# Performance work log

Measured on AMD Instinct MI355X. Metric: run time of the kernel, lower is better.

The kernel has to match this reference:

```python
import jax, jax.numpy as jnp
import numpy as np

B, N, D = 2, 2048, 1024
H, HD = 16, 64
BASE = 10000.0
INIT_STD = 0.02


def apply_rope(x, base=BASE):
    """Rotary embedding on the last dim; seq axis is axis 1.

    Works for q of shape (b, n, h, d) and k of shape (b, n, d).
    """
    d = x.shape[-1]
    n = x.shape[1]
    half = d // 2
    inv_freq = 1.0 / (base ** (jnp.arange(half, dtype=jnp.float32) / half))
    ang = jnp.arange(n, dtype=jnp.float32)[:, None] * inv_freq  # (n, d/2)
    extra = x.ndim - 3  # axes between seq axis and feature axis
    ang = ang.reshape((n,) + (1,) * extra + (half,))
    cos, sin = jnp.cos(ang), jnp.sin(ang)
    x1, x2 = jnp.split(x, 2, axis=-1)
    return jnp.concatenate([x1 * cos - x2 * sin, x2 * cos + x1 * sin], axis=-1)


def setup_inputs() -> dict:
    key = jax.random.key(0)
    kx, k1, k2, k3, k4 = jax.random.split(key, 5)
    x = jax.random.normal(kx, (B, N, D), dtype=jnp.float32)
    Wq = jax.random.normal(k1, (D, H * HD), dtype=jnp.float32) * INIT_STD
    Wkv = jax.random.normal(k2, (D, 2 * HD), dtype=jnp.float32) * INIT_STD
    Wkvh = jax.random.normal(k3, (D, 2 * H), dtype=jnp.float32) * INIT_STD
    Wo = jax.random.normal(k4, (H * HD, D), dtype=jnp.float32) * INIT_STD
    return {"x": x, "Wq": Wq, "Wkv": Wkv, "Wkvh": Wkvh, "Wo": Wo}


def reference(x, Wq, Wkv, Wkvh, Wo):
    b, n, d = x.shape
    q = (x @ Wq).reshape(b, n, H, HD)          # (b,n,h,hd)
    kv = x @ Wkv                                # (b,n,2*hd)
    kv_head = jax.nn.sigmoid(x @ Wkvh)          # (b,n,2*h)
    k, v = jnp.split(kv, 2, axis=-1)            # each (b,n,hd)
    k_head, v_head = jnp.split(kv_head, 2, axis=-1)  # each (b,n,h)

    # LRPE (rotary) on q and on the shared low-rank k
    q = apply_rope(q)
    k = apply_rope(k)

    # outer-product expansion: (b,n,h) x (b,n,hd) -> (b,n,h,hd)
    k = jnp.einsum('bnh,bnd->bnhd', k_head, k)
    v = jnp.einsum('bnh,bnd->bnhd', v_head, v)

    # causal softmax attention, scale = 1/sqrt(head_dim)
    scale = 1.0 / np.sqrt(HD)
    scores = jnp.einsum('bqhd,bkhd->bhqk', q, k) * scale
    mask = jnp.tril(jnp.ones((n, n), dtype=bool))
    scores = jnp.where(mask, scores, jnp.finfo(scores.dtype).min)
    p = jax.nn.softmax(scores, axis=-1)
    out = jnp.einsum('bhqk,bkhd->bqhd', p, v)   # (b,n,h,hd)

    out = out.reshape(b, n, H * HD)
    return out @ Wo
```

## Files before the change

### kernel.cpp

```cpp
#include <hip/hip_runtime.h>

typedef unsigned short u16;
typedef unsigned int u32;
typedef __attribute__((ext_vector_type(8))) short short8;
typedef __attribute__((ext_vector_type(4))) float f32x4;
typedef __attribute__((ext_vector_type(4))) u32 u32x4;
typedef __attribute__((ext_vector_type(2))) u32 u32x2;
typedef __attribute__((ext_vector_type(4))) u16 u16x4;

constexpr int B_ = 2, N_ = 2048, H_ = 16;
constexpr int ROWS = B_ * N_;
constexpr float LOG2E = 1.44269504088896f;

__device__ __forceinline__ float bf2f(u16 u){ union{u32 u; float f;} v; v.u = ((u32)u)<<16; return v.f; }
__device__ __forceinline__ u16 f2bf(float f){
  union{float f; u32 u;} v; v.f = f;
  u32 u = v.u; u += 0x7fffu + ((u>>16)&1u);
  return (u16)(u>>16);
}
__device__ __forceinline__ u32 cvtpk(float lo, float hi){
  u32 r; asm("v_cvt_pk_bf16_f32 %0, %1, %2" : "=v"(r) : "v"(lo), "v"(hi)); return r;
}

__global__ __launch_bounds__(256) void k_setup(const float* __restrict__ x, u16* __restrict__ xb,
                                               float2* __restrict__ tab,
                                               const float* __restrict__ Wq, const float* __restrict__ Wo,
                                               u16* __restrict__ WqT, u16* __restrict__ WoT,
                                               const float* __restrict__ Wkv, const float* __restrict__ Wkvh,
                                               u16* __restrict__ WkvT){
  __shared__ float T[64*65];
  int bid = blockIdx.x, tid = threadIdx.x;
  if (bid < 4096){
    int i = (bid*256 + tid)*4;
    f32x4 v = *(const f32x4*)(x + i);
    u16x4 o; o[0]=f2bf(v[0]); o[1]=f2bf(v[1]); o[2]=f2bf(v[2]); o[3]=f2bf(v[3]);
    *(u16x4*)(xb + i) = o;
    return;
  }
  if (bid < 4352){
    int idx = (bid-4096)*256 + tid;
    int i = idx & 31, n = idx >> 5;
    float ang = (float)n * exp2f(-(float)i * 0.4152410118609203f);
    tab[idx] = make_float2(cosf(ang), sinf(ang));
    return;
  }
  if (bid < 4864){
    int m = (bid - 4352) >> 8;
    const float* in = m ? Wo : Wq;
    u16* out = m ? WoT : WqT;
    int t2 = (bid - 4352) & 255;
    int n0 = (t2 & 15) << 6, k0 = (t2 >> 4) << 6;
    #pragma unroll
    for (int s=0; s<4; ++s){
      int chunk = tid + s*256, r = chunk >> 4, c4 = (chunk & 15) << 2;
      *(f32x4*)(&T[r*65 + c4]) = *(const f32x4*)(&in[(size_t)(k0 + r)*1024 + n0 + c4]);
    }
    __syncthreads();
    #pragma unroll
    for (int s=0; s<2; ++s){
      int chunk = tid + s*256, d = chunk >> 3, c8 = (chunk & 7) << 3;
      u16x4 o1, o2;
      #pragma unroll
      for (int j=0; j<4; ++j){ o1[j] = f2bf(T[(c8+j)*65 + d]); o2[j] = f2bf(T[(c8+4+j)*65 + d]); }
      *(u16x4*)(&out[(size_t)(n0 + d)*1024 + k0 + c8])     = o1;
      *(u16x4*)(&out[(size_t)(n0 + d)*1024 + k0 + c8 + 4]) = o2;
    }
    return;
  }
  {
    int idx = (bid - 4864)*256 + tid;
    int n = idx >> 10, k = idx & 1023;
    float v = 0.f;
    if (n < 128)      v = Wkv[k*128 + n];
    else if (n < 160) v = Wkvh[k*32 + (n-128)];
    WkvT[idx] = f2bf(v);
  }
}

__global__ __launch_bounds__(256) void k_gemm_bt(const u16* __restrict__ A, const u16* __restrict__ Bt,
                                                 float* __restrict__ C, int M, int N, int K){
  __shared__ u16 As[64*72];
  __shared__ u16 Bs[64*72];
  int ntile = N >> 6;
  int m0 = (blockIdx.x / ntile) << 6;
  int n0 = (blockIdx.x % ntile) << 6;
  int tid = threadIdx.x;
  int w = tid >> 6, l = tid & 63, lr = l & 15, lc = l >> 4;
  int wm = (w >> 1) * 32, wn = (w & 1) * 32;
  f32x4 acc[2][2] = {};
  for (int kt = 0; kt < K; kt += 64){
    __syncthreads();
    #pragma unroll
    for (int s = 0; s < 2; ++s){
      int chunk = tid + s*256;
      int r = chunk >> 3, c8 = (chunk & 7) << 3;
      *(u32x4*)(&As[r*72 + c8]) = *(const u32x4*)(&A[(size_t)(m0 + r)*K + kt + c8]);
      *(u32x4*)(&Bs[r*72 + c8]) = *(const u32x4*)(&Bt[(size_t)(n0 + r)*K + kt + c8]);
    }
    __syncthreads();
    short8 af[2][2], bfr[2][2];
    #pragma unroll
    for (int mf=0; mf<2; ++mf)
      #pragma unroll
      for (int c=0; c<2; ++c)
        af[mf][c] = *(const short8*)(&As[(wm + mf*16 + lr)*72 + c*32 + lc*8]);
    #pragma unroll
    for (int nf=0; nf<2; ++nf)
      #pragma unroll
      for (int c=0; c<2; ++c)
        bfr[nf][c] = *(const short8*)(&Bs[(wn + nf*16 + lr)*72 + c*32 + lc*8]);
    #pragma unroll
    for (int mf=0; mf<2; ++mf)
      #pragma unroll
      for (int nf=0; nf<2; ++nf)
        #pragma unroll
        for (int c=0; c<2; ++c)
          acc[mf][nf] = __builtin_amdgcn_mfma_f32_16x16x32_bf16(af[mf][c], bfr[nf][c], acc[mf][nf], 0,0,0);
  }
  #pragma unroll
  for (int mf=0; mf<2; ++mf)
    #pragma unroll
    for (int nf=0; nf<2; ++nf)
      #pragma unroll
      for (int r=0; r<4; ++r)
        C[(size_t)(m0 + wm + mf*16 + lc*4 + r)*N + n0 + wn + nf*16 + lr] = acc[mf][nf][r];
}

template<int MODE>
__global__ __launch_bounds__(256) void k_gemm_mn(const u16* __restrict__ A, const u16* __restrict__ Bt,
                                                 void* __restrict__ Cv, const float2* __restrict__ tab,
                                                 int M, int N, int K){
  __shared__ u16 As[128*64];
  __shared__ u16 Bs[64*64];
  int ntile = N >> 6;
  int m0 = (blockIdx.x / ntile) << 7;
  int n0 = (blockIdx.x % ntile) << 6;
  int tid = threadIdx.x;
  int l = tid & 63, lr = l & 15, lc = l >> 4;
  int w = tid >> 6;
  int wm = w * 32;
  f32x4 acc[2][4] = {};
  for (int kt = 0; kt < K; kt += 64){
    __syncthreads();
    #pragma unroll
    for (int s = 0; s < 4; ++s){
      int chunk = tid + s*256, r = chunk >> 3, c8 = (chunk & 7) << 3;
      __builtin_amdgcn_global_load_lds(
        (const __attribute__((address_space(1))) u32*)(&A[(size_t)(m0 + r)*K + kt + c8]),
        (__attribute__((address_space(3))) u32*)(&As[r*64 + c8]), 16, 0, 0);
    }
    #pragma unroll
    for (int s = 0; s < 2; ++s){
      int chunk = tid + s*256, r = chunk >> 3, c8 = (chunk & 7) << 3;
      __builtin_amdgcn_global_load_lds(
        (const __attribute__((address_space(1))) u32*)(&Bt[(size_t)(n0 + r)*K + kt + c8]),
        (__attribute__((address_space(3))) u32*)(&Bs[r*64 + c8]), 16, 0, 0);
    }
    __syncthreads();
    short8 af[2][2], bfr[4][2];
    #pragma unroll
    for (int m=0; m<2; ++m)
      #pragma unroll
      for (int c=0; c<2; ++c)
        af[m][c] = *(const short8*)(&As[(wm + m*16 + lr)*64 + c*32 + lc*8]);
    #pragma unroll
    for (int n=0; n<4; ++n)
      #pragma unroll
      for (int c=0; c<2; ++c)
        bfr[n][c] = *(const short8*)(&Bs[(n*16 + lr)*64 + c*32 + lc*8]);
    __builtin_amdgcn_s_setprio(1);
    #pragma unroll
    for (int m=0; m<2; ++m)
      #pragma unroll
      for (int n=0; n<4; ++n)
        #pragma unroll
        for (int c=0; c<2; ++c)
          acc[m][n] = __builtin_amdgcn_mfma_f32_16x16x32_bf16(af[m][c], bfr[n][c], acc[m][n], 0,0,0);
    __builtin_amdgcn_s_setprio(0);
  }
  if constexpr (MODE == 0){
    float* C = (float*)Cv;
    #pragma unroll
    for (int m=0; m<2; ++m)
      #pragma unroll
      for (int n=0; n<4; ++n)
        #pragma unroll
        for (int r=0; r<4; ++r)
          C[(size_t)(m0 + wm + m*16 + lc*4 + r)*N + n0 + n*16 + lr] = acc[m][n][r];
  } else {
    u16* C = (u16*)Cv;
    #pragma unroll
    for (int m=0; m<2; ++m){
      int grow = m0 + wm + m*16 + lc*4;
      #pragma unroll
      for (int nf=0; nf<2; ++nf){
        int i = nf*16 + lr;
        #pragma unroll
        for (int r=0; r<4; ++r){
          float2 cs = tab[(size_t)((grow + r) & (N_-1))*32 + i];
          float x1 = acc[m][nf][r], x2 = acc[m][nf+2][r];
          C[(size_t)(grow + r)*N + n0 + i]      = f2bf(0.125f*(x1*cs.x - x2*cs.y));
          C[(size_t)(grow + r)*N + n0 + i + 32] = f2bf(0.125f*(x2*cs.x + x1*cs.y));
        }
      }
    }
  }
}

__global__ __launch_bounds__(256) void k_postproc2(const float* __restrict__ proj, const float2* __restrict__ tab,
                                                   u16* __restrict__ k_rope, float* __restrict__ k_head,
                                                   float* __restrict__ v_head, u16* __restrict__ vt){
  __shared__ u16 Tv[64*72];
  int n0 = blockIdx.x << 6;
  int b = n0 >> 11;
  int tid = threadIdx.x;
  #pragma unroll
  for (int s=0; s<4; ++s){
    int chunk = tid + s*256, r = chunk >> 4, c4 = (chunk & 15) << 2;
    f32x4 v = *(const f32x4*)(&proj[(size_t)(n0+r)*192 + 64 + c4]);
    u16x4 o; o[0]=f2bf(v[0]); o[1]=f2bf(v[1]); o[2]=f2bf(v[2]); o[3]=f2bf(v[3]);
    *(u16x4*)(&Tv[r*72 + c4]) = o;
  }
  int wv = tid>>6, t = tid&63;
  for (int rr = wv; rr < 64; rr += 4){
    int row = n0 + rr, n = row & (N_-1);
    const float* p = proj + (size_t)row*192;
    if (t < 32){
      float hv = 1.f/(1.f + __expf(-p[128 + t]));
      if (t < 16) k_head[((size_t)b*16 + t)*N_ + n] = hv * LOG2E;
      else        v_head[((size_t)b*16 + (t-16))*N_ + n] = hv;
      float2 cs = tab[n*32 + t];
      float k1 = p[t], k2 = p[32 + t];
      k_rope[(size_t)row*64 + t]      = f2bf(k1*cs.x - k2*cs.y);
      k_rope[(size_t)row*64 + 32 + t] = f2bf(k2*cs.x + k1*cs.y);
    }
  }
  __syncthreads();
  int nb = n0 & (N_-1);
  #pragma unroll
  for (int s=0; s<2; ++s){
    int chunk = tid + s*256, d = chunk>>3, c8 = (chunk&7)<<3;
    u32x4 o; u16* op = (u16*)&o;
    #pragma unroll
    for (int j=0; j<8; ++j) op[j] = Tv[(c8+j)*72 + d];
    *(u32x4*)(&vt[((size_t)b*64 + d)*N_ + nb + c8]) = o;
  }
}

__global__ __launch_bounds__(256, 4) void k_attn6(const u16* __restrict__ q_bf, const u16* __restrict__ k_rp,
                                                  const u16* __restrict__ vt, const float* __restrict__ k_hd,
                                                  const float* __restrict__ v_hd, u16* __restrict__ attn_o){
  __shared__ u16 Ks[64*72];
  __shared__ u16 Vts[64*72];
  __shared__ u16 Ps[4][16*72];
  __shared__ float g_s[128];
  int z = blockIdx.x;
  int qt = 31 - (z >> 5);
  int h = z & 15, b = (z >> 4) & 1;
  int tid = threadIdx.x, w = tid>>6, l = tid&63, lr = l&15, lc = l>>4;
  size_t rowbase = (size_t)b*N_;
  size_t qoff = (rowbase + qt*64 + w*16 + lr)*1024 + h*64;
  short8 qf0 = *(const short8*)(&q_bf[qoff + lc*8]);
  short8 qf1 = *(const short8*)(&q_bf[qoff + 32 + lc*8]);
  const float* gkp = k_hd + ((size_t)b*16 + h)*N_;
  const float* gvp = v_hd + ((size_t)b*16 + h)*N_;
  u32x4 kr[2], vr[2]; float gr;
  auto issue = [&](int t){
    int kg0 = t << 6;
    #pragma unroll
    for (int s=0; s<2; ++s){
      int chunk = tid + s*256, r = chunk>>3, c8 = (chunk&7)<<3;
      kr[s] = *(const u32x4*)(&k_rp[(rowbase + kg0 + r)*64 + c8]);
      vr[s] = *(const u32x4*)(&vt[((size_t)b*64 + r)*N_ + kg0 + c8]);
    }
    gr = (tid < 64) ? gkp[kg0 + tid] : ((tid < 128) ? gvp[kg0 + tid - 64] : 0.f);
  };
  float lsum = 0.f;
  f32x4 o[4] = {};
  issue(0);
  for (int t = 0; t <= qt; ++t){
    int kg0 = t << 6;
    __syncthreads();
    #pragma unroll
    for (int s=0; s<2; ++s){
      int chunk = tid + s*256, r = chunk>>3, c8 = (chunk&7)<<3;
      *(u32x4*)(&Ks[r*72 + c8])  = kr[s];
      *(u32x4*)(&Vts[r*72 + c8]) = vr[s];
    }
    if (tid < 128) g_s[tid] = gr;
    if (t < qt) issue(t+1);
    __syncthreads();
    f32x4 s4[4];
    __builtin_amdgcn_s_setprio(1);
    #pragma unroll
    for (int nf=0; nf<4; ++nf){
      short8 kf0 = *(const short8*)(&Ks[(nf*16+lr)*72 + lc*8]);
      short8 kf1 = *(const short8*)(&Ks[(nf*16+lr)*72 + 32 + lc*8]);
      f32x4 zz = {};
      zz = __builtin_amdgcn_mfma_f32_16x16x32_bf16(kf0, qf0, zz, 0,0,0);
      s4[nf] = __builtin_amdgcn_mfma_f32_16x16x32_bf16(kf1, qf1, zz, 0,0,0);
    }
    __builtin_amdgcn_s_setprio(0);
    #pragma unroll
    for (int nf=0; nf<4; ++nf){
      f32x4 gkv = *(const f32x4*)(&g_s[nf*16 + lc*4]);
      #pragma unroll
      for (int r=0; r<4; ++r) s4[nf][r] *= gkv[r];
    }
    if (t == qt){
      int qg = qt*64 + w*16 + lr;
      #pragma unroll
      for (int nf=0; nf<4; ++nf)
        #pragma unroll
        for (int r=0; r<4; ++r)
          if (kg0 + nf*16 + lc*4 + r > qg) s4[nf][r] = -1e30f;
    }
    #pragma unroll
    for (int nf=0; nf<4; ++nf)
      #pragma unroll
      for (int r=0; r<4; ++r){ s4[nf][r] = exp2f(s4[nf][r]); lsum += s4[nf][r]; }
    #pragma unroll
    for (int nf=0; nf<4; ++nf){
      f32x4 gvv = *(const f32x4*)(&g_s[64 + nf*16 + lc*4]);
      u32 lo = cvtpk(s4[nf][0]*gvv[0], s4[nf][1]*gvv[1]);
      u32 hi = cvtpk(s4[nf][2]*gvv[2], s4[nf][3]*gvv[3]);
      *(u32x2*)(&Ps[w][lr*72 + nf*16 + lc*4]) = (u32x2){lo, hi};
    }
    asm volatile("s_waitcnt lgkmcnt(0)" ::: "memory");
    __builtin_amdgcn_sched_barrier(0);
    short8 pf0 = *(const short8*)(&Ps[w][lr*72 + lc*8]);
    short8 pf1 = *(const short8*)(&Ps[w][lr*72 + 32 + lc*8]);
    __builtin_amdgcn_s_setprio(1);
    #pragma unroll
    for (int nf=0; nf<4; ++nf){
      short8 vf0 = *(const short8*)(&Vts[(nf*16+lr)*72 + lc*8]);
      short8 vf1 = *(const short8*)(&Vts[(nf*16+lr)*72 + 32 + lc*8]);
      o[nf] = __builtin_amdgcn_mfma_f32_16x16x32_bf16(pf0, vf0, o[nf], 0,0,0);
      o[nf] = __builtin_amdgcn_mfma_f32_16x16x32_bf16(pf1, vf1, o[nf], 0,0,0);
    }
    __builtin_amdgcn_s_setprio(0);
  }
  lsum += __shfl_xor(lsum, 16);
  lsum += __shfl_xor(lsum, 32);
  f32x4 lv;
  #pragma unroll
  for (int r=0; r<4; ++r) lv[r] = __builtin_amdgcn_rcpf(__shfl(lsum, lc*4 + r, 16));
  #pragma unroll
  for (int nf=0; nf<4; ++nf)
    #pragma unroll
    for (int r=0; r<4; ++r)
      attn_o[(rowbase + qt*64 + w*16 + lc*4 + r)*1024 + h*64 + nf*16 + lr] = f2bf(o[nf][r] * lv[r]);
}

extern "C" void kernel_launch(void* const* d_in, const int* in_sizes, int n_in,
                              void* d_out, int out_size, void* d_ws, size_t ws_size,
                              hipStream_t stream){
  const float* x    = (const float*)d_in[0];
  const float* Wq   = (const float*)d_in[1];
  const float* Wkv  = (const float*)d_in[2];
  const float* Wkvh = (const float*)d_in[3];
  const float* Wo   = (const float*)d_in[4];
  float* out = (float*)d_out;

  char* p = (char*)d_ws;
  u16* xb      = (u16*)p;   p += (size_t)ROWS*1024*2;
  u16* WqT     = (u16*)p;   p += (size_t)1024*1024*2;
  u16* WoT     = (u16*)p;   p += (size_t)1024*1024*2;
  u16* WkvT    = (u16*)p;   p += (size_t)192*1024*2;
  float* proj  = (float*)p; p += (size_t)ROWS*192*4;
  u16* q_bf    = (u16*)p;   p += (size_t)ROWS*1024*2;
  u16* k_rp    = (u16*)p;   p += (size_t)ROWS*64*2;
  u16* vt      = (u16*)p;   p += (size_t)B_*64*N_*2;
  float* k_hd  = (float*)p; p += (size_t)B_*H_*N_*4;
  float* v_hd  = (float*)p; p += (size_t)B_*H_*N_*4;
  float2* tab  = (float2*)p; p += (size_t)N_*32*8;
  u16* attn_o  = xb;

  k_setup<<<4096 + 256 + 512 + 768, 256, 0, stream>>>(x, xb, tab, Wq, Wo, WqT, WoT, Wkv, Wkvh, WkvT);
  k_gemm_mn<1><<<(ROWS/128)*(1024/64), 256, 0, stream>>>(xb, WqT, q_bf, tab, ROWS, 1024, 1024);
  k_gemm_bt<<<(ROWS/64)*(192/64), 256, 0, stream>>>(xb, WkvT, proj, ROWS, 192, 1024);
  k_postproc2<<<ROWS/64, 256, 0, stream>>>(proj, tab, k_rp, k_hd, v_hd, vt);
  k_attn6<<<B_*H_*32, 256, 0, stream>>>(q_bf, k_rp, vt, k_hd, v_hd, attn_o);
  k_gemm_mn<0><<<(ROWS/128)*(1024/64), 256, 0, stream>>>(attn_o, WoT, out, nullptr, ROWS, 1024, 1024);
}
```

Before: 125.0 us.

## Split causal attention KV range across two blocks and fuse KV projection into Q GEMM

Attention is split along the key dimension into two blocks per query tile, each writing unnormalized bf16 partial outputs and row sums. A new combine kernel adds the partials and normalizes them. The KV/gate projection weights are appended to the Q weight matrix so a single GEMM produces both Q (with rope) and the fp32 projection, removing the separate small GEMM. The aim is to shorten the causal tail and cut launches, at the cost of extra partial-buffer traffic, an additional kernel, and bf16 rounding of the partials.

```diff
diff --git a/kernel.cpp b/kernel.cpp
--- a/kernel.cpp
+++ b/kernel.cpp
@@ -77,58 +77,10 @@
   }
 }
 
-__global__ __launch_bounds__(256) void k_gemm_bt(const u16* __restrict__ A, const u16* __restrict__ Bt,
-                                                 float* __restrict__ C, int M, int N, int K){
-  __shared__ u16 As[64*72];
-  __shared__ u16 Bs[64*72];
-  int ntile = N >> 6;
-  int m0 = (blockIdx.x / ntile) << 6;
-  int n0 = (blockIdx.x % ntile) << 6;
-  int tid = threadIdx.x;
-  int w = tid >> 6, l = tid & 63, lr = l & 15, lc = l >> 4;
-  int wm = (w >> 1) * 32, wn = (w & 1) * 32;
-  f32x4 acc[2][2] = {};
-  for (int kt = 0; kt < K; kt += 64){
-    __syncthreads();
-    #pragma unroll
-    for (int s = 0; s < 2; ++s){
-      int chunk = tid + s*256;
-      int r = chunk >> 3, c8 = (chunk & 7) << 3;
-      *(u32x4*)(&As[r*72 + c8]) = *(const u32x4*)(&A[(size_t)(m0 + r)*K + kt + c8]);
-      *(u32x4*)(&Bs[r*72 + c8]) = *(const u32x4*)(&Bt[(size_t)(n0 + r)*K + kt + c8]);
-    }
-    __syncthreads();
-    short8 af[2][2], bfr[2][2];
-    #pragma unroll
-    for (int mf=0; mf<2; ++mf)
-      #pragma unroll
-      for (int c=0; c<2; ++c)
-        af[mf][c] = *(const short8*)(&As[(wm + mf*16 + lr)*72 + c*32 + lc*8]);
-    #pragma unroll
-    for (int nf=0; nf<2; ++nf)
-      #pragma unroll
-      for (int c=0; c<2; ++c)
-        bfr[nf][c] = *(const short8*)(&Bs[(wn + nf*16 + lr)*72 + c*32 + lc*8]);
-    #pragma unroll
-    for (int mf=0; mf<2; ++mf)
-      #pragma unroll
-      for (int nf=0; nf<2; ++nf)
-        #pragma unroll
-        for (int c=0; c<2; ++c)
-          acc[mf][nf] = __builtin_amdgcn_mfma_f32_16x16x32_bf16(af[mf][c], bfr[nf][c], acc[mf][nf], 0,0,0);
-  }
-  #pragma unroll
-  for (int mf=0; mf<2; ++mf)
-    #pragma unroll
-    for (int nf=0; nf<2; ++nf)
-      #pragma unroll
-      for (int r=0; r<4; ++r)
-        C[(size_t)(m0 + wm + mf*16 + lc*4 + r)*N + n0 + wn + nf*16 + lr] = acc[mf][nf][r];
-}
-
 template<int MODE>
 __global__ __launch_bounds__(256) void k_gemm_mn(const u16* __restrict__ A, const u16* __restrict__ Bt,
-                                                 void* __restrict__ Cv, const float2* __restrict__ tab,
+                                                 void* __restrict__ Cv, float* __restrict__ proj,
+                                                 const float2* __restrict__ tab,
                                                  int M, int N, int K){
   __shared__ u16 As[128*64];
   __shared__ u16 Bs[64*64];
@@ -188,21 +140,32 @@
         for (int r=0; r<4; ++r)
           C[(size_t)(m0 + wm + m*16 + lc*4 + r)*N + n0 + n*16 + lr] = acc[m][n][r];
   } else {
-    u16* C = (u16*)Cv;
-    #pragma unroll
-    for (int m=0; m<2; ++m){
-      int grow = m0 + wm + m*16 + lc*4;
-      #pragma unroll
-      for (int nf=0; nf<2; ++nf){
-        int i = nf*16 + lr;
-        #pragma unroll
-        for (int r=0; r<4; ++r){
-          float2 cs = tab[(size_t)((grow + r) & (N_-1))*32 + i];
-          float x1 = acc[m][nf][r], x2 = acc[m][nf+2][r];
-          C[(size_t)(grow + r)*N + n0 + i]      = f2bf(0.125f*(x1*cs.x - x2*cs.y));
-          C[(size_t)(grow + r)*N + n0 + i + 32] = f2bf(0.125f*(x2*cs.x + x1*cs.y));
+    if (n0 < 1024){
+      u16* C = (u16*)Cv;
+      #pragma unroll
+      for (int m=0; m<2; ++m){
+        int grow = m0 + wm + m*16 + lc*4;
+        #pragma unroll
+        for (int nf=0; nf<2; ++nf){
+          int i = nf*16 + lr;
+          #pragma unroll
+          for (int r=0; r<4; ++r){
+            float2 cs = tab[(size_t)((grow + r) & (N_-1))*32 + i];
+            float x1 = acc[m][nf][r], x2 = acc[m][nf+2][r];
+            C[(size_t)(grow + r)*1024 + n0 + i]      = f2bf(0.125f*(x1*cs.x - x2*cs.y));
+            C[(size_t)(grow + r)*1024 + n0 + i + 32] = f2bf(0.125f*(x2*cs.x + x1*cs.y));
+          }
         }
       }
+    } else {
+      int pc = n0 - 1024;
+      #pragma unroll
+      for (int m=0; m<2; ++m)
+        #pragma unroll
+        for (int n=0; n<4; ++n)
+          #pragma unroll
+          for (int r=0; r<4; ++r)
+            proj[(size_t)(m0 + wm + m*16 + lc*4 + r)*192 + pc + n*16 + lr] = acc[m][n][r];
     }
   }
 }
@@ -247,17 +210,27 @@
   }
 }
 
-__global__ __launch_bounds__(256, 4) void k_attn6(const u16* __restrict__ q_bf, const u16* __restrict__ k_rp,
+__global__ __launch_bounds__(256, 4) void k_attn7(const u16* __restrict__ q_bf, const u16* __restrict__ k_rp,
                                                   const u16* __restrict__ vt, const float* __restrict__ k_hd,
-                                                  const float* __restrict__ v_hd, u16* __restrict__ attn_o){
+                                                  const float* __restrict__ v_hd,
+                                                  u16* __restrict__ o_part, float* __restrict__ l_part){
   __shared__ u16 Ks[64*72];
   __shared__ u16 Vts[64*72];
   __shared__ u16 Ps[4][16*72];
   __shared__ float g_s[128];
   int z = blockIdx.x;
-  int qt = 31 - (z >> 5);
-  int h = z & 15, b = (z >> 4) & 1;
+  int pidx = z >> 1, sp = z & 1;
+  int qt = 31 - (pidx >> 5);
+  int h = pidx & 15, b = (pidx >> 4) & 1;
+  int h0 = (qt + 1) >> 1;
+  int t0 = sp ? h0 : 0, t1 = sp ? (qt + 1) : h0;
   int tid = threadIdx.x, w = tid>>6, l = tid&63, lr = l&15, lc = l>>4;
+  if (t0 >= t1){
+    u16* op = o_part + (size_t)z*4096;
+    for (int i = tid; i < 512; i += 256) *(u32x4*)(op + i*8) = (u32x4){0,0,0,0};
+    if (tid < 64) l_part[z*64 + tid] = 0.f;
+    return;
+  }
   size_t rowbase = (size_t)b*N_;
   size_t qoff = (rowbase + qt*64 + w*16 + lr)*1024 + h*64;
   short8 qf0 = *(const short8*)(&q_bf[qoff + lc*8]);
@@ -277,8 +250,8 @@
   };
   float lsum = 0.f;
   f32x4 o[4] = {};
-  issue(0);
-  for (int t = 0; t <= qt; ++t){
+  issue(t0);
+  for (int t = t0; t < t1; ++t){
     int kg0 = t << 6;
     __syncthreads();
     #pragma unroll
@@ -288,7 +261,7 @@
       *(u32x4*)(&Vts[r*72 + c8]) = vr[s];
     }
     if (tid < 128) g_s[tid] = gr;
-    if (t < qt) issue(t+1);
+    if (t + 1 < t1) issue(t+1);
     __syncthreads();
     f32x4 s4[4];
     __builtin_amdgcn_s_setprio(1);
@@ -342,14 +315,38 @@
   }
   lsum += __shfl_xor(lsum, 16);
   lsum += __shfl_xor(lsum, 32);
-  f32x4 lv;
-  #pragma unroll
-  for (int r=0; r<4; ++r) lv[r] = __builtin_amdgcn_rcpf(__shfl(lsum, lc*4 + r, 16));
+  if (lc == 0) l_part[z*64 + w*16 + lr] = lsum;
+  u16* op = o_part + (size_t)z*4096;
   #pragma unroll
   for (int nf=0; nf<4; ++nf)
     #pragma unroll
     for (int r=0; r<4; ++r)
-      attn_o[(rowbase + qt*64 + w*16 + lc*4 + r)*1024 + h*64 + nf*16 + lr] = f2bf(o[nf][r] * lv[r]);
+      op[(w*16 + lc*4 + r)*64 + nf*16 + lr] = f2bf(o[nf][r]);
+}
+
+__global__ __launch_bounds__(256) void k_comb(const u16* __restrict__ o_part, const float* __restrict__ l_part,
+                                              u16* __restrict__ attn_o){
+  int z2 = blockIdx.x;
+  int qt = 31 - (z2 >> 5), h = z2 & 15, b = (z2 >> 4) & 1;
+  int tid = threadIdx.x;
+  int q = tid >> 2, c16 = (tid & 3) << 4;
+  size_t base0 = (size_t)(2*z2)*4096 + q*64 + c16;
+  float lv = l_part[(2*z2)*64 + q] + l_part[(2*z2+1)*64 + q];
+  float rl = __builtin_amdgcn_rcpf(lv);
+  union U8 { u32x4 v; u16 s[8]; };
+  U8 a0, a1, b0, b1, r0, r1;
+  a0.v = *(const u32x4*)(o_part + base0);
+  a1.v = *(const u32x4*)(o_part + base0 + 8);
+  b0.v = *(const u32x4*)(o_part + base0 + 4096);
+  b1.v = *(const u32x4*)(o_part + base0 + 4096 + 8);
+  #pragma unroll
+  for (int j=0; j<8; ++j){
+    r0.s[j] = f2bf((bf2f(a0.s[j]) + bf2f(b0.s[j])) * rl);
+    r1.s[j] = f2bf((bf2f(a1.s[j]) + bf2f(b1.s[j])) * rl);
+  }
+  u16* outp = attn_o + ((size_t)(b*N_ + qt*64 + q))*1024 + h*64 + c16;
+  *(u32x4*)outp = r0.v;
+  *(u32x4*)(outp + 8) = r1.v;
 }
 
 extern "C" void kernel_launch(void* const* d_in, const int* in_sizes, int n_in,
@@ -364,9 +361,8 @@
 
   char* p = (char*)d_ws;
   u16* xb      = (u16*)p;   p += (size_t)ROWS*1024*2;
-  u16* WqT     = (u16*)p;   p += (size_t)1024*1024*2;
+  u16* WT      = (u16*)p;   p += (size_t)1216*1024*2;
   u16* WoT     = (u16*)p;   p += (size_t)1024*1024*2;
-  u16* WkvT    = (u16*)p;   p += (size_t)192*1024*2;
   float* proj  = (float*)p; p += (size_t)ROWS*192*4;
   u16* q_bf    = (u16*)p;   p += (size_t)ROWS*1024*2;
   u16* k_rp    = (u16*)p;   p += (size_t)ROWS*64*2;
@@ -374,12 +370,15 @@
   float* k_hd  = (float*)p; p += (size_t)B_*H_*N_*4;
   float* v_hd  = (float*)p; p += (size_t)B_*H_*N_*4;
   float2* tab  = (float2*)p; p += (size_t)N_*32*8;
+  u16* o_part  = (u16*)p;   p += (size_t)2048*4096*2;
+  float* l_part= (float*)p; p += (size_t)2048*64*4;
   u16* attn_o  = xb;
 
-  k_setup<<<4096 + 256 + 512 + 768, 256, 0, stream>>>(x, xb, tab, Wq, Wo, WqT, WoT, Wkv, Wkvh, WkvT);
-  k_gemm_mn<1><<<(ROWS/128)*(1024/64), 256, 0, stream>>>(xb, WqT, q_bf, tab, ROWS, 1024, 1024);
-  k_gemm_bt<<<(ROWS/64)*(192/64), 256, 0, stream>>>(xb, WkvT, proj, ROWS, 192, 1024);
+  k_setup<<<4096 + 256 + 512 + 768, 256, 0, stream>>>(x, xb, tab, Wq, Wo, WT, WoT,
+                                                      Wkv, Wkvh, WT + (size_t)1024*1024);
+  k_gemm_mn<1><<<(ROWS/128)*(1216/64), 256, 0, stream>>>(xb, WT, q_bf, proj, tab, ROWS, 1216, 1024);
   k_postproc2<<<ROWS/64, 256, 0, stream>>>(proj, tab, k_rp, k_hd, v_hd, vt);
-  k_attn6<<<B_*H_*32, 256, 0, stream>>>(q_bf, k_rp, vt, k_hd, v_hd, attn_o);
-  k_gemm_mn<0><<<(ROWS/128)*(1024/64), 256, 0, stream>>>(attn_o, WoT, out, nullptr, ROWS, 1024, 1024);
-}
+  k_attn7<<<2048, 256, 0, stream>>>(q_bf, k_rp, vt, k_hd, v_hd, o_part, l_part);
+  k_comb<<<1024, 256, 0, stream>>>(o_part, l_part, attn_o);
+  k_gemm_mn<0><<<(ROWS/128)*(1024/64), 256, 0, stream>>>(attn_o, WoT, out, nullptr, nullptr, ROWS, 1024, 1024);
+}
```

New measurement: 113.9 us. 8.9% less time.
